# Kernel optimization log

Hardware: AMD Instinct MI355X
Metric: run time of the kernel (lower is better)

Reference implementation:

```python
import jax, jax.numpy as jnp
import numpy as np


def setup_inputs() -> dict:
    key = jax.random.key(0)
    ks = jax.random.split(key, 5)
    dim = 512
    B, D, H, W = 2, 32, 32, 32
    x = jax.random.normal(ks[0], (B, D, H, W, dim), dtype=jnp.float32)
    # torch nn.Linear-style params stored as [in, out]
    W_qkv = jax.random.normal(ks[1], (dim, 3 * dim), dtype=jnp.float32) * (dim ** -0.5)
    b_qkv = jnp.zeros((3 * dim,), dtype=jnp.float32)
    W_proj = jax.random.normal(ks[2], (dim, dim), dtype=jnp.float32) * (dim ** -0.5)
    b_proj = jnp.zeros((dim,), dtype=jnp.float32)
    return {"x": x, "W_qkv": W_qkv, "b_qkv": b_qkv, "W_proj": W_proj, "b_proj": b_proj}


def reference(x, W_qkv, b_qkv, W_proj, b_proj):
    num_heads = 8
    ws = 4
    B, D, H, W, C = x.shape
    head_dim = C // num_heads
    scale = head_dim ** -0.5
    nd, nh, nw = D // ws, H // ws, W // ws
    num_windows = nd * nh * nw
    T = ws ** 3  # tokens per window

    # window partition: [B, nd, ws, nh, ws, nw, ws, C] -> [B*nwin, T, C]
    xw = x.reshape(B, nd, ws, nh, ws, nw, ws, C)
    xw = xw.transpose(0, 1, 3, 5, 2, 4, 6, 7).reshape(B * num_windows, T, C)

    qkv = xw @ W_qkv + b_qkv  # [N, T, 3C]
    qkv = qkv.reshape(-1, T, 3, num_heads, head_dim).transpose(2, 0, 3, 1, 4)
    q, k, v = qkv[0], qkv[1], qkv[2]  # each [N, heads, T, hd]

    attn = jnp.einsum("nhtd,nhsd->nhts", q, k) * scale
    attn = jnp.clip(attn, -10000.0, 10000.0)
    attn = jax.nn.softmax(attn, axis=-1)
    attn = jnp.nan_to_num(attn, nan=0.0)

    out = jnp.einsum("nhts,nhsd->nhtd", attn, v)  # [N, heads, T, hd]
    out = out.transpose(0, 2, 1, 3).reshape(-1, T, C)
    out = out @ W_proj + b_proj

    # window reverse
    out = out.reshape(B, nd, nh, nw, ws, ws, ws, C)
    out = out.transpose(0, 1, 4, 2, 5, 3, 6, 7).reshape(B, D, H, W, C)
    return out
```

## Files before the change

kernel.cpp:

```cpp
#include <hip/hip_runtime.h>

typedef unsigned int u32;
typedef unsigned short u16;
typedef __attribute__((ext_vector_type(4))) float f32x4;
typedef __attribute__((ext_vector_type(8))) short bf16x8;
typedef __attribute__((ext_vector_type(4))) u32 u32x4;

__device__ __forceinline__ u16 f2bf(float f) {
  u32 u = __builtin_bit_cast(u32, f);
  u = u + 0x7FFFu + ((u >> 16) & 1u);
  return (u16)(u >> 16);
}
__device__ __forceinline__ u32 pack2(float a, float b) {
  return (u32)f2bf(a) | ((u32)f2bf(b) << 16);
}
__device__ __forceinline__ bf16x8 pack8(f32x4 a, f32x4 b) {
  union { u32 w[4]; bf16x8 v; } u;
  u.w[0] = pack2(a[0], a[1]); u.w[1] = pack2(a[2], a[3]);
  u.w[2] = pack2(b[0], b[1]); u.w[3] = pack2(b[2], b[3]);
  return u.v;
}

#define MFMA(a, b, c) __builtin_amdgcn_mfma_f32_16x16x32_bf16((a), (b), (c), 0, 0, 0)

__device__ __forceinline__ bf16x8 lds_frag(const char* buf, int rowBytes, int row, int kByte) {
  return *(const bf16x8*)(buf + row * rowBytes + (kByte ^ ((row & 7) << 4)));
}

__device__ __forceinline__ int tok_global(int blk, int t) {
  int b = blk >> 9, r = blk & 511;
  int wd = r >> 6, wh = (r >> 3) & 7, ww = r & 7;
  int d = wd * 4 + (t >> 4);
  int h = wh * 4 + ((t >> 2) & 3);
  int w = ww * 4 + (t & 3);
  return ((b * 32 + d) * 32 + h) * 32 + w;
}

__global__ void prep_weights(const float* __restrict__ wq, const float* __restrict__ wp,
                             u16* __restrict__ wtq, u16* __restrict__ wtp) {
  int idx = blockIdx.x * 512 + threadIdx.x;
  if (idx < 512 * 1536) {
    int i = idx / 1536, o = idx % 1536;
    int c = i & 31;
    int lane = (c >> 3) * 16 + (o & 15);
    wtq[((size_t)(o >> 4) * 16 + (i >> 5)) * 512 + lane * 8 + (c & 7)] = f2bf(wq[idx]);
  } else {
    int j = idx - 512 * 1536;
    int i = j >> 9, o = j & 511;
    int c = i & 31;
    int lane = (c >> 3) * 16 + (o & 15);
    wtp[((size_t)(o >> 4) * 16 + (i >> 5)) * 512 + lane * 8 + (c & 7)] = f2bf(wp[j]);
  }
}

#define GEMM_PASS_AB(WLANE, SMEMBASE)                                         \
  {                                                                           \
    bf16x8 wfs[3][4];                                                         \
    _Pragma("unroll") for (int i = 0; i < 4; ++i)                             \
        wfs[0][i] = *(const bf16x8*)((WLANE) + (i * 16 + 0) * 512);           \
    _Pragma("unroll") for (int i = 0; i < 4; ++i)                             \
        wfs[1][i] = *(const bf16x8*)((WLANE) + (i * 16 + 1) * 512);           \
    _Pragma("unroll") for (int ks = 0; ks < 16; ++ks) {                       \
      if (ks < 14) {                                                          \
        _Pragma("unroll") for (int i = 0; i < 4; ++i)                         \
            wfs[(ks + 2) % 3][i] =                                            \
                *(const bf16x8*)((WLANE) + (i * 16 + ks + 2) * 512);          \
      }                                                                       \
      bf16x8 bx[4];                                                           \
      const int kByte = ks * 64 + g * 16;                                     \
      _Pragma("unroll") for (int j = 0; j < 4; ++j)                           \
          bx[j] = lds_frag((SMEMBASE), 1024, j * 16 + lr, kByte);             \
      __builtin_amdgcn_s_setprio(1);                                          \
      _Pragma("unroll") for (int i = 0; i < 4; ++i)                           \
        _Pragma("unroll") for (int j = 0; j < 4; ++j)                         \
            acc[i][j] = MFMA(wfs[ks % 3][i], bx[j], acc[i][j]);               \
      __builtin_amdgcn_s_setprio(0);                                          \
    }                                                                         \
  }
#define GEMM_PASS_BA(WLANE, SMEMBASE)                                         \
  {                                                                           \
    bf16x8 wfs[3][4];                                                         \
    _Pragma("unroll") for (int i = 0; i < 4; ++i)                             \
        wfs[0][i] = *(const bf16x8*)((WLANE) + (i * 16 + 0) * 512);           \
    _Pragma("unroll") for (int i = 0; i < 4; ++i)                             \
        wfs[1][i] = *(const bf16x8*)((WLANE) + (i * 16 + 1) * 512);           \
    _Pragma("unroll") for (int ks = 0; ks < 16; ++ks) {                       \
      if (ks < 14) {                                                          \
        _Pragma("unroll") for (int i = 0; i < 4; ++i)                         \
            wfs[(ks + 2) % 3][i] =                                            \
                *(const bf16x8*)((WLANE) + (i * 16 + ks + 2) * 512);          \
      }                                                                       \
      bf16x8 bx[4];                                                           \
      const int kByte = ks * 64 + g * 16;                                     \
      _Pragma("unroll") for (int j = 0; j < 4; ++j)                           \
          bx[j] = lds_frag((SMEMBASE), 1024, j * 16 + lr, kByte);             \
      __builtin_amdgcn_s_setprio(1);                                          \
      _Pragma("unroll") for (int i = 0; i < 4; ++i)                           \
        _Pragma("unroll") for (int j = 0; j < 4; ++j)                         \
            acc[i][j] = MFMA(bx[i], wfs[ks % 3][j], acc[i][j]);               \
      __builtin_amdgcn_s_setprio(0);                                          \
    }                                                                         \
  }

__global__ __launch_bounds__(512, 2) void fused_win_attn(
    const float* __restrict__ x, const float* __restrict__ bq, const float* __restrict__ bp,
    const u16* __restrict__ wtq, const u16* __restrict__ wtp, float* __restrict__ out) {
  __shared__ char smem[65536];
  const int tid = threadIdx.x;
  const int wv = tid >> 6;
  const int l  = tid & 63;
  const int lr = l & 15;
  const int g  = l >> 4;
  const int blk = blockIdx.x;

  {
    const int st = tid >> 3, seg = tid & 7;
    const float* xs = x + (size_t)tok_global(blk, st) * 512 + seg * 64;
    char* dst = smem + st * 1024;
    const int swz = (st & 7) << 4;
    float4 f[16];
#pragma unroll
    for (int i = 0; i < 16; ++i) f[i] = ((const float4*)xs)[i];
#pragma unroll
    for (int i = 0; i < 8; ++i) {
      const int ic = (i + seg) & 7;
      u32x4 w = {pack2(f[2 * ic].x, f[2 * ic].y),         pack2(f[2 * ic].z, f[2 * ic].w),
                 pack2(f[2 * ic + 1].x, f[2 * ic + 1].y), pack2(f[2 * ic + 1].z, f[2 * ic + 1].w)};
      *(u32x4*)(dst + ((seg * 128 + ic * 16) ^ swz)) = w;
    }
  }
  __syncthreads();

  const u16* wqL = wtq + ((size_t)wv * 4 * 16) * 512 + l * 8;
  const u16* wkL = wqL + (size_t)512 * 512;
  const u16* wvL = wqL + (size_t)1024 * 512;
  const u16* wpL = wtp + ((size_t)wv * 4 * 16) * 512 + l * 8;

  bf16x8 qp[4][2], ka[4][2], pb[4][2], va[4][2];
  f32x4 acc[4][4];

#pragma unroll
  for (int i = 0; i < 4; ++i)
#pragma unroll
    for (int j = 0; j < 4; ++j) acc[i][j] = (f32x4)0.f;
  GEMM_PASS_AB(wqL, smem);
#pragma unroll
  for (int i = 0; i < 4; ++i) {
    const int och = wv * 64 + i * 16 + g * 4;
    f32x4 qb = {bq[och], bq[och + 1], bq[och + 2], bq[och + 3]};
#pragma unroll
    for (int j = 0; j < 4; ++j) acc[i][j] += qb;
  }
#pragma unroll
  for (int j = 0; j < 4; ++j)
#pragma unroll
    for (int kb = 0; kb < 2; ++kb)
      qp[j][kb] = pack8(acc[2 * kb][j], acc[2 * kb + 1][j]);

#pragma unroll
  for (int i = 0; i < 4; ++i)
#pragma unroll
    for (int j = 0; j < 4; ++j) acc[i][j] = (f32x4)0.f;
  GEMM_PASS_AB(wkL, smem);
#pragma unroll
  for (int i = 0; i < 4; ++i) {
    const int och = 512 + wv * 64 + i * 16 + g * 4;
    f32x4 kb = {bq[och], bq[och + 1], bq[och + 2], bq[och + 3]};
#pragma unroll
    for (int j = 0; j < 4; ++j) acc[i][j] += kb;
  }
#pragma unroll
  for (int m = 0; m < 4; ++m)
#pragma unroll
    for (int kb = 0; kb < 2; ++kb)
      ka[m][kb] = pack8(acc[2 * kb][m], acc[2 * kb + 1][m]);

  {
    f32x4 sacc[4][4];
#pragma unroll
    for (int m = 0; m < 4; ++m)
#pragma unroll
      for (int j = 0; j < 4; ++j) {
        f32x4 a = (f32x4)0.f;
        a = MFMA(ka[m][0], qp[j][0], a);
        sacc[m][j] = MFMA(ka[m][1], qp[j][1], a);
      }
#pragma unroll
    for (int m = 0; m < 4; ++m)
#pragma unroll
      for (int j = 0; j < 4; ++j)
#pragma unroll
        for (int r = 0; r < 4; ++r) {
          float v = sacc[m][j][r] * 0.125f;
          sacc[m][j][r] = fminf(fmaxf(v, -10000.f), 10000.f);
        }
    float mx[4], sm[4];
#pragma unroll
    for (int j = 0; j < 4; ++j) {
      float a0 = fmaxf(fmaxf(sacc[0][j][0], sacc[0][j][1]), fmaxf(sacc[0][j][2], sacc[0][j][3]));
      float a1 = fmaxf(fmaxf(sacc[1][j][0], sacc[1][j][1]), fmaxf(sacc[1][j][2], sacc[1][j][3]));
      float a2 = fmaxf(fmaxf(sacc[2][j][0], sacc[2][j][1]), fmaxf(sacc[2][j][2], sacc[2][j][3]));
      float a3 = fmaxf(fmaxf(sacc[3][j][0], sacc[3][j][1]), fmaxf(sacc[3][j][2], sacc[3][j][3]));
      mx[j] = fmaxf(fmaxf(a0, a1), fmaxf(a2, a3));
    }
#pragma unroll
    for (int j = 0; j < 4; ++j) mx[j] = fmaxf(mx[j], __shfl_xor(mx[j], 16));
#pragma unroll
    for (int j = 0; j < 4; ++j) mx[j] = fmaxf(mx[j], __shfl_xor(mx[j], 32));
#pragma unroll
    for (int j = 0; j < 4; ++j) {
      float s0 = 0.f;
#pragma unroll
      for (int m = 0; m < 4; ++m)
#pragma unroll
        for (int r = 0; r < 4; ++r) {
          float p = __expf(sacc[m][j][r] - mx[j]);
          sacc[m][j][r] = p;
          s0 += p;
        }
      sm[j] = s0;
    }
#pragma unroll
    for (int j = 0; j < 4; ++j) sm[j] += __shfl_xor(sm[j], 16);
#pragma unroll
    for (int j = 0; j < 4; ++j) sm[j] += __shfl_xor(sm[j], 32);
#pragma unroll
    for (int j = 0; j < 4; ++j) {
      float inv = 1.f / sm[j];
#pragma unroll
      for (int kb = 0; kb < 2; ++kb)
        pb[j][kb] = pack8(sacc[2 * kb][j] * inv, sacc[2 * kb + 1][j] * inv);
    }
  }

#pragma unroll
  for (int i = 0; i < 4; ++i)
#pragma unroll
    for (int j = 0; j < 4; ++j) acc[i][j] = (f32x4)0.f;
  GEMM_PASS_BA(wvL, smem);
#pragma unroll
  for (int ni = 0; ni < 4; ++ni) {
    float bv = bq[1024 + wv * 64 + ni * 16 + lr];
#pragma unroll
    for (int ti = 0; ti < 4; ++ti) acc[ti][ni] += (f32x4)bv;
#pragma unroll
    for (int kb = 0; kb < 2; ++kb)
      va[ni][kb] = pack8(acc[2 * kb][ni], acc[2 * kb + 1][ni]);
  }

  __syncthreads();

#pragma unroll
  for (int ni = 0; ni < 4; ++ni)
#pragma unroll
    for (int j = 0; j < 4; ++j) {
      f32x4 a = (f32x4)0.f;
      a = MFMA(va[ni][0], pb[j][0], a);
      a = MFMA(va[ni][1], pb[j][1], a);
      int t = j * 16 + lr;
      int cb = (wv * 64 + ni * 16 + g * 4) * 2;
      int swz = (t & 7) << 4;
      *(u32*)(smem + t * 1024 + (cb ^ swz))       = pack2(a[0], a[1]);
      *(u32*)(smem + t * 1024 + ((cb + 4) ^ swz)) = pack2(a[2], a[3]);
    }
  __syncthreads();

#pragma unroll
  for (int i = 0; i < 4; ++i)
#pragma unroll
    for (int j = 0; j < 4; ++j) acc[i][j] = (f32x4)0.f;
  GEMM_PASS_AB(wpL, smem);
#pragma unroll
  for (int mi = 0; mi < 4; ++mi) {
    const int och = wv * 64 + mi * 16 + g * 4;
    float b0 = bp[och], b1 = bp[och + 1], b2 = bp[och + 2], b3 = bp[och + 3];
#pragma unroll
    for (int tj = 0; tj < 4; ++tj) {
      int t = tj * 16 + lr;
      f32x4 v = acc[mi][tj];
      float4 o;
      o.x = v[0] + b0; o.y = v[1] + b1; o.z = v[2] + b2; o.w = v[3] + b3;
      *(float4*)(out + (size_t)tok_global(blk, t) * 512 + och) = o;
    }
  }
}

extern "C" void kernel_launch(void* const* d_in, const int* in_sizes, int n_in,
                              void* d_out, int out_size, void* d_ws, size_t ws_size,
                              hipStream_t stream) {
  const float* x  = (const float*)d_in[0];
  const float* wq = (const float*)d_in[1];
  const float* bq = (const float*)d_in[2];
  const float* wp = (const float*)d_in[3];
  const float* bp = (const float*)d_in[4];
  float* out = (float*)d_out;
  u16* wtq = (u16*)d_ws;
  u16* wtp = wtq + 512 * 1536;

  prep_weights<<<2048, 512, 0, stream>>>(wq, wp, wtq, wtp);
  fused_win_attn<<<1024, 512, 0, stream>>>(x, bq, bp, wtq, wtp, out);
}
```

Measured before the change: 226.8 us.

## Double-buffer LDS B-fragments in GEMM passes and stage output stores through LDS

The GEMM macros now prefetch the next k-step's LDS activation fragments into a double buffer, so LDS read latency overlaps with the current MFMA batch. The epilogue adds the bias in registers, then writes the output tile to swizzled shared memory in two halves of 32 tokens. Each wave then stores full contiguous 1 KB token rows to global memory instead of scattered 16-byte pieces. This costs more registers, which may hurt occupancy under the 512x2 launch bounds, and adds extra barriers.

```diff
diff --git a/kernel.cpp b/kernel.cpp
--- a/kernel.cpp
+++ b/kernel.cpp
@@ -55,49 +55,57 @@
 
 #define GEMM_PASS_AB(WLANE, SMEMBASE)                                         \
   {                                                                           \
-    bf16x8 wfs[3][4];                                                         \
+    bf16x8 wfs[3][4], bxs[2][4];                                              \
     _Pragma("unroll") for (int i = 0; i < 4; ++i)                             \
         wfs[0][i] = *(const bf16x8*)((WLANE) + (i * 16 + 0) * 512);           \
     _Pragma("unroll") for (int i = 0; i < 4; ++i)                             \
         wfs[1][i] = *(const bf16x8*)((WLANE) + (i * 16 + 1) * 512);           \
+    _Pragma("unroll") for (int j = 0; j < 4; ++j)                             \
+        bxs[0][j] = lds_frag((SMEMBASE), 1024, j * 16 + lr, g * 16);          \
     _Pragma("unroll") for (int ks = 0; ks < 16; ++ks) {                       \
+      if (ks < 15) {                                                          \
+        const int kb1 = (ks + 1) * 64 + g * 16;                               \
+        _Pragma("unroll") for (int j = 0; j < 4; ++j)                         \
+            bxs[(ks + 1) & 1][j] =                                            \
+                lds_frag((SMEMBASE), 1024, j * 16 + lr, kb1);                 \
+      }                                                                       \
       if (ks < 14) {                                                          \
         _Pragma("unroll") for (int i = 0; i < 4; ++i)                         \
             wfs[(ks + 2) % 3][i] =                                            \
                 *(const bf16x8*)((WLANE) + (i * 16 + ks + 2) * 512);          \
       }                                                                       \
-      bf16x8 bx[4];                                                           \
-      const int kByte = ks * 64 + g * 16;                                     \
-      _Pragma("unroll") for (int j = 0; j < 4; ++j)                           \
-          bx[j] = lds_frag((SMEMBASE), 1024, j * 16 + lr, kByte);             \
       __builtin_amdgcn_s_setprio(1);                                          \
       _Pragma("unroll") for (int i = 0; i < 4; ++i)                           \
         _Pragma("unroll") for (int j = 0; j < 4; ++j)                         \
-            acc[i][j] = MFMA(wfs[ks % 3][i], bx[j], acc[i][j]);               \
+            acc[i][j] = MFMA(wfs[ks % 3][i], bxs[ks & 1][j], acc[i][j]);      \
       __builtin_amdgcn_s_setprio(0);                                          \
     }                                                                         \
   }
 #define GEMM_PASS_BA(WLANE, SMEMBASE)                                         \
   {                                                                           \
-    bf16x8 wfs[3][4];                                                         \
+    bf16x8 wfs[3][4], bxs[2][4];                                              \
     _Pragma("unroll") for (int i = 0; i < 4; ++i)                             \
         wfs[0][i] = *(const bf16x8*)((WLANE) + (i * 16 + 0) * 512);           \
     _Pragma("unroll") for (int i = 0; i < 4; ++i)                             \
         wfs[1][i] = *(const bf16x8*)((WLANE) + (i * 16 + 1) * 512);           \
+    _Pragma("unroll") for (int j = 0; j < 4; ++j)                             \
+        bxs[0][j] = lds_frag((SMEMBASE), 1024, j * 16 + lr, g * 16);          \
     _Pragma("unroll") for (int ks = 0; ks < 16; ++ks) {                       \
+      if (ks < 15) {                                                          \
+        const int kb1 = (ks + 1) * 64 + g * 16;                               \
+        _Pragma("unroll") for (int j = 0; j < 4; ++j)                         \
+            bxs[(ks + 1) & 1][j] =                                            \
+                lds_frag((SMEMBASE), 1024, j * 16 + lr, kb1);                 \
+      }                                                                       \
       if (ks < 14) {                                                          \
         _Pragma("unroll") for (int i = 0; i < 4; ++i)                         \
             wfs[(ks + 2) % 3][i] =                                            \
                 *(const bf16x8*)((WLANE) + (i * 16 + ks + 2) * 512);          \
       }                                                                       \
-      bf16x8 bx[4];                                                           \
-      const int kByte = ks * 64 + g * 16;                                     \
-      _Pragma("unroll") for (int j = 0; j < 4; ++j)                           \
-          bx[j] = lds_frag((SMEMBASE), 1024, j * 16 + lr, kByte);             \
       __builtin_amdgcn_s_setprio(1);                                          \
       _Pragma("unroll") for (int i = 0; i < 4; ++i)                           \
         _Pragma("unroll") for (int j = 0; j < 4; ++j)                         \
-            acc[i][j] = MFMA(bx[i], wfs[ks % 3][j], acc[i][j]);               \
+            acc[i][j] = MFMA(bxs[ks & 1][i], wfs[ks % 3][j], acc[i][j]);      \
       __builtin_amdgcn_s_setprio(0);                                          \
     }                                                                         \
   }
@@ -273,14 +281,32 @@
 #pragma unroll
   for (int mi = 0; mi < 4; ++mi) {
     const int och = wv * 64 + mi * 16 + g * 4;
-    float b0 = bp[och], b1 = bp[och + 1], b2 = bp[och + 2], b3 = bp[och + 3];
-#pragma unroll
-    for (int tj = 0; tj < 4; ++tj) {
-      int t = tj * 16 + lr;
-      f32x4 v = acc[mi][tj];
-      float4 o;
-      o.x = v[0] + b0; o.y = v[1] + b1; o.z = v[2] + b2; o.w = v[3] + b3;
-      *(float4*)(out + (size_t)tok_global(blk, t) * 512 + och) = o;
+    f32x4 bb = {bp[och], bp[och + 1], bp[och + 2], bp[och + 3]};
+#pragma unroll
+    for (int tj = 0; tj < 4; ++tj) acc[mi][tj] += bb;
+  }
+
+#pragma unroll
+  for (int th = 0; th < 2; ++th) {
+    __syncthreads();
+#pragma unroll
+    for (int mi = 0; mi < 4; ++mi)
+#pragma unroll
+      for (int jj = 0; jj < 2; ++jj) {
+        const int tj = th * 2 + jj;
+        const int tl = (tj * 16 + lr) & 31;
+        const int ochb = (wv * 64 + mi * 16 + g * 4) * 4;
+        *(f32x4*)(smem + tl * 2048 + (ochb ^ ((tl & 7) << 4))) = acc[mi][tj];
+      }
+    __syncthreads();
+#pragma unroll
+    for (int it = 0; it < 8; ++it) {
+      const int task = it * 8 + wv;
+      const int tl = task >> 1;
+      const int hf = task & 1;
+      const int ochb = hf * 1024 + l * 16;
+      f32x4 v = *(const f32x4*)(smem + tl * 2048 + (ochb ^ ((tl & 7) << 4)));
+      *(f32x4*)(out + (size_t)tok_global(blk, th * 32 + tl) * 512 + hf * 256 + l * 4) = v;
     }
   }
 }
```

Result: no change. 222.6 us, median of 2 (-1.9%).
